# Optimization experiments

Measured on AMD Instinct MI355X. Metric: run time of the kernel, lower is better.

Reference implementation:

```python
import jax, jax.numpy as jnp
import numpy as np
from functools import partial

FRAME_RATE = 100
MIN_BPM = 55.0
MAX_BPM = 215.0
THRESHOLD = 0.05
TRANSITION_LAMBDA = 100.0  # madmom-style exponential tempo-change penalty
NEG = jnp.float32(-1e9)


def _build_dbn():
    """Bar-pointer DBN: one block of `tau` phase states per tempo interval tau."""
    min_int = int(round(60.0 * FRAME_RATE / MAX_BPM))
    max_int = int(round(60.0 * FRAME_RATE / MIN_BPM))
    intervals = np.arange(min_int, max_int + 1)              # (T_tempi,)
    state_positions = np.concatenate([np.arange(t) for t in intervals])  # (S,)
    first_idx = np.cumsum(intervals) - intervals             # pos-0 state per tempo
    last_idx = np.cumsum(intervals) - 1                      # last state per tempo
    # exponential tempo-transition distribution, row-normalized in log space
    ratio = intervals[None, :].astype(np.float64) / intervals[:, None]
    raw = -TRANSITION_LAMBDA * np.abs(ratio - 1.0)
    trans_log = raw - np.log(np.exp(raw - raw.max(1, keepdims=True)).sum(1, keepdims=True)) - raw.max(1, keepdims=True)
    return (
        jnp.asarray(state_positions == 0),                    # pos0_mask (S,) bool
        jnp.asarray(first_idx, dtype=jnp.int32),
        jnp.asarray(last_idx, dtype=jnp.int32),
        jnp.asarray(trans_log, dtype=jnp.float32),            # (T_tempi, T_tempi)
    )


def setup_inputs() -> dict:
    key = jax.random.key(0)
    logit = jax.random.normal(key, (4, 6000), dtype=jnp.float32)
    return {"logit": logit}


@jax.jit
def reference(logit):
    pos0_mask, first_idx, last_idx, trans_log = _build_dbn()
    S = pos0_mask.shape[0]
    B, T = logit.shape

    beat_lp = jax.nn.log_sigmoid(logit)      # (B, T)
    nonbeat_lp = jax.nn.log_sigmoid(-logit)  # (B, T)

    def emission(b_t, nb_t):
        # (B, S): beat log-prob on phase-0 states, non-beat elsewhere
        return jnp.where(pos0_mask[None, :], b_t[:, None], nb_t[:, None])

    # ---- Viterbi forward pass with backpointers ----
    def step(delta, xs):
        b_t, nb_t = xs
        prev_last = delta[:, last_idx]                         # (B, T_tempi)
        cand = prev_last[:, :, None] + trans_log[None, :, :]   # (B, from, to)
        from_beat = cand.max(axis=1)                           # (B, T_tempi)
        bp_beat = last_idx[cand.argmax(axis=1)]                # (B, T_tempi)
        # within-tempo advance: state s comes from s-1 (blocks are contiguous)
        shifted = jnp.concatenate(
            [jnp.full((B, 1), NEG, delta.dtype), delta[:, :-1]], axis=1)
        combined = shifted.at[:, first_idx].set(from_beat)
        new_delta = combined + emission(b_t, nb_t)
        bp = jnp.broadcast_to(jnp.arange(S, dtype=jnp.int32) - 1, (B, S))
        bp = bp.at[:, first_idx].set(bp_beat)
        return new_delta, bp

    delta0 = emission(beat_lp[:, 0], nonbeat_lp[:, 0]) - jnp.log(jnp.float32(S))
    xs = (beat_lp[:, 1:].T, nonbeat_lp[:, 1:].T)               # each (T-1, B)
    delta_final, bps = jax.lax.scan(step, delta0, xs)          # bps: (T-1, B, S)

    # ---- backtrack ----
    final_state = jnp.argmax(delta_final, axis=1).astype(jnp.int32)  # (B,)

    def back(state, bp_t):
        prev = jnp.take_along_axis(bp_t, state[:, None], axis=1)[:, 0]
        return prev, state

    state0, ys = jax.lax.scan(back, final_state, bps, reverse=True)
    path = jnp.concatenate([state0[None, :], ys], axis=0)      # (T, B) state ids

    on_beat = pos0_mask[path].T                                # (B, T)
    act = jax.nn.sigmoid(logit)
    beat_mask = on_beat & (act >= jnp.float32(THRESHOLD))
    return beat_mask.astype(jnp.float32)                       # 1.0 at beat frames
```

## Files before the change

### kernel.cpp

```cpp
#include <hip/hip_runtime.h>
#include <math.h>

#define NTAU 82
#define TMIN 28
#define S_TOT 5617
#define TF 6000
#define BATCH 4
#define WMAX 28
#define AP 84
#define LP 96
#define GP 88
#define NTHREADS 1024
#define NCHUNK 215
#define CHUNK_G (WMAX * GP)
#define NPOS 41
#define FLAG_STRIDE 64

#define TRANS_OFF 0
#define BLP_OFF   8192
#define NBLP_OFF  32768
#define AH_OFF    57344
#define FLAG_OFF  (AH_OFF + BATCH * NCHUNK * CHUNK_G)
#define RESV_OFF  (FLAG_OFF + 8 * FLAG_STRIDE)
#define RESI_OFF  (RESV_OFF + 8)

typedef float v2f __attribute__((ext_vector_type(2)));

__device__ __forceinline__ int first_of(int b) { return b * (55 + b) / 2; }

__device__ __forceinline__ float logsig(float x) {
    return -(fmaxf(-x, 0.0f) + log1pf(expf(-fabsf(x))));
}

__global__ void k_trans(float* __restrict__ ws) {
    int i = blockIdx.x;
    int j = threadIdx.x;
    __shared__ double sh[128];
    double raw = 0.0, e = 0.0;
    double ti = 28.0 + (double)i;
    if (j < NTAU) {
        double tj = 28.0 + (double)j;
        raw = -100.0 * fabs(tj / ti - 1.0);
        e = exp(raw);
    }
    sh[j] = e;
    __syncthreads();
    for (int st = 64; st > 0; st >>= 1) {
        if (j < st) sh[j] += sh[j + st];
        __syncthreads();
    }
    double lse = log(sh[0]);
    if (j < NTAU) ws[TRANS_OFF + i * NTAU + j] = (float)(raw - lse);
}

__global__ void k_emis(const float* __restrict__ logit, float* __restrict__ ws,
                       float* __restrict__ out) {
    int idx = blockIdx.x * blockDim.x + threadIdx.x;
    if (idx < BATCH * TF) {
        float x = logit[idx];
        ws[BLP_OFF + idx]  = logsig(x);
        ws[NBLP_OFF + idx] = logsig(-x);
        out[idx] = 0.0f;
    }
}

__global__ void k_flags(int* __restrict__ flags) {
    int i = blockIdx.x * blockDim.x + threadIdx.x;
    if (i < 8 * FLAG_STRIDE) flags[i] = 0;
}

__global__ void k_ahpad(float* __restrict__ Ah) {
    int i = blockIdx.x * blockDim.x + threadIdx.x;
    const int total = BATCH * NCHUNK * WMAX * 2 * 3;
    if (i < total) {
        int c3 = i % 3; int rest = i / 3;
        int par = rest & 1; rest >>= 1;
        int row = rest % WMAX; rest /= WMAX;
        int chunk = rest % NCHUNK; int bb = rest / NCHUNK;
        Ah[(size_t)bb * NCHUNK * CHUNK_G + (size_t)chunk * CHUNK_G
           + row * GP + par * 44 + 41 + c3] = -1.0e30f;
    }
}

__global__ __attribute__((amdgpu_flat_work_group_size(NTHREADS, NTHREADS),
                          amdgpu_waves_per_eu(4, 4),
                          amdgpu_num_vgpr(128)))
void k_viterbi(const float* __restrict__ logit,
               const float* __restrict__ transg,
               const float* __restrict__ blp_all,
               const float* __restrict__ nblp_all,
               float* __restrict__ Ah_all,
               int*   __restrict__ flags,
               float* __restrict__ resv,
               int*   __restrict__ resi,
               float* __restrict__ out) {
    const int tid = threadIdx.x;
    const int b   = blockIdx.x >> 1;
    const int h   = blockIdx.x & 1;

    const float* blp  = blp_all  + b * TF;
    const float* nblp = nblp_all + b * TF;
    float* Ah = Ah_all + (size_t)b * (NCHUNK * CHUNK_G);
    int* flagOut = flags + (b * 2 + h) * FLAG_STRIDE;
    int* flagIn  = flags + (b * 2 + (1 - h)) * FLAG_STRIDE;

    __shared__ float V[2832];
    __shared__ __align__(16) float A_lds[WMAX * LP];
    __shared__ __align__(16) float fb[CHUNK_G];
    __shared__ __align__(16) float win_nb[4][WMAX];
    __shared__ __align__(16) float win_b[4][WMAX];
    __shared__ float wv[16];
    __shared__ int   wi[16];
    __shared__ int   sstate;

    const int iseg = tid & 3;
    const int jpp  = (tid >> 2) % 21;
    const int tg   = tid / 84;
    const bool p2act = (tid < 1008);
    const int p0s = iseg * 12;
    const int j0 = 4 * jpp + h;
    const bool j1v = (jpp < 20);
    const int j1 = j1v ? (4 * jpp + 2 + h) : j0;

    float trO0[12], trO1[12], trP0[12], trP1[12];
#pragma unroll
    for (int k = 0; k < 12; ++k) {
        trO0[k] = -1.0e30f; trO1[k] = -1.0e30f;
        trP0[k] = -1.0e30f; trP1[k] = -1.0e30f;
    }
    if (p2act) {
#pragma unroll
        for (int k = 0; k < 12; ++k) {
            const int p = p0s + k;
            if (p <= 40) {
                const int iO = 2 * p + h, iP = 2 * p + 1 - h;
                trO0[k] = transg[iO * NTAU + j0];
                trP0[k] = transg[iP * NTAU + j0];
                if (j1v) {
                    trO1[k] = transg[iO * NTAU + j1];
                    trP1[k] = transg[iP * NTAU + j1];
                }
            }
        }
    }

    const bool ract = (tid < 1008);
    const int ro = ract ? (tid / 36) : 27;
    const int sp = tid % 36;
    const bool rv2 = ract && (sp < 5);
    const int pA = sp, pB = sp + 36;
    const int tauA = 28 + 2 * pA + h, tauB = 28 + 2 * pB + h;
    const int foA = pA * (27 + pA + h), foB = pB * (27 + pB + h);
    int rrA = ro, rrB = ro;

    const int NF_TOT = NPOS * (NPOS - 1 + h);
    int nrR[2], nrFo[2], nrTau[2];
    bool nrV[2];
#pragma unroll
    for (int q = 0; q < 2; ++q) {
        const int f = tid + q * NTHREADS;
        nrV[q] = (f < NF_TOT);
        nrR[q] = 28; nrFo[q] = 0; nrTau[q] = 109;
        if (nrV[q]) {
            int lo = 0, hi = NPOS - 1;
            while (lo < hi) { int mid = (lo + hi + 1) >> 1;
                              if (mid * (mid - 1 + h) <= f) lo = mid; else hi = mid - 1; }
            const int m = f - lo * (lo - 1 + h);
            nrR[q]   = TMIN + m;
            nrFo[q]  = lo * (27 + lo + h);
            nrTau[q] = TMIN + 2 * lo + h;
        }
    }

    const float logS = (float)log((double)S_TOT);
    const float b0 = blp[0], n0 = nblp[0];
    const int SOWN = NPOS * (68 + h);
    for (int g = tid; g < SOWN; g += NTHREADS) {
        int lo = 0, hi = NPOS - 1;
        while (lo < hi) { int mid = (lo + hi + 1) >> 1;
                          if (mid * (27 + mid + h) <= g) lo = mid; else hi = mid - 1; }
        const int tau = TMIN + 2 * lo + h;
        const int r = g - lo * (27 + lo + h);
        V[g] = ((r == tau - 1) ? b0 : n0) - logS;
    }

    for (int idx = tid; idx < WMAX * LP; idx += NTHREADS) A_lds[idx] = -1.0e30f;

    auto winload = [&](int cc) {
        if (cc < NCHUNK && tid < WMAX) {
            int gt = 1 + cc * WMAX + tid;
            win_nb[cc & 3][tid] = (gt < TF) ? nblp[gt] : 0.0f;
            win_b [cc & 3][tid] = (gt < TF) ? blp[gt]  : 0.0f;
        }
    };
    winload(0);
    winload(1);
    __syncthreads();

#define PH2P(av, aw, t0a, t0b, t1a, t1b) { \
    float x0 = (av) + (t0a); float y0 = (aw) + (t0b); \
    m0 = fmaxf(fmaxf(m0, x0), y0); \
    float x1 = (av) + (t1a); float y1 = (aw) + (t1b); \
    m1 = fmaxf(fmaxf(m1, x1), y1); }

    float cvA = 0.0f, cvB = 0.0f;
    float pm0[3], pm1[3];
    for (int c = 0; c < NCHUNK; ++c) {
        const int buf = c & 3;
        float* AhC = Ah + (size_t)c * CHUNK_G;

        cvA = ract ? V[foA + rrA] : 0.0f;
        cvB = rv2  ? V[foB + rrB] : 0.0f;
        for (int tt = 0; tt < ro; ++tt) {
            const float w = win_nb[buf][tt];
            cvA += w; cvB += w;
        }
        if (ract) {
            A_lds[ro * LP + h * 48 + pA] = cvA;
            __hip_atomic_store(&AhC[ro * GP + h * 44 + pA], cvA,
                               __ATOMIC_RELAXED, __HIP_MEMORY_SCOPE_AGENT);
            if (rv2) {
                A_lds[ro * LP + h * 48 + pB] = cvB;
                __hip_atomic_store(&AhC[ro * GP + h * 44 + pB], cvB,
                                   __ATOMIC_RELAXED, __HIP_MEMORY_SCOPE_AGENT);
            }
        }
        winload(c + 2);
        __syncthreads();

        if (tid == 0)
            __hip_atomic_store(flagOut, c + 1, __ATOMIC_RELAXED, __HIP_MEMORY_SCOPE_AGENT);

        if (p2act) {
#pragma unroll
            for (int u = 0; u < 3; ++u) {
                const int tl = tg + 12 * u;
                float m0 = -INFINITY, m1 = -INFINITY;
                if (tl < WMAX) {
                    const float4* ar4 = (const float4*)&A_lds[tl * LP + h * 48 + p0s];
                    const float4 a0 = ar4[0], a1 = ar4[1], a2 = ar4[2];
                    PH2P(a0.x, a0.y, trO0[0], trO0[1], trO1[0], trO1[1])
                    PH2P(a0.z, a0.w, trO0[2], trO0[3], trO1[2], trO1[3])
                    PH2P(a1.x, a1.y, trO0[4], trO0[5], trO1[4], trO1[5])
                    PH2P(a1.z, a1.w, trO0[6], trO0[7], trO1[6], trO1[7])
                    PH2P(a2.x, a2.y, trO0[8], trO0[9], trO1[8], trO1[9])
                    PH2P(a2.z, a2.w, trO0[10], trO0[11], trO1[10], trO1[11])
                }
                pm0[u] = m0; pm1[u] = m1;
            }
        }

        {
            const int a0 = nrFo[0] + nrR[0];
            const int a1 = nrV[1] ? (nrFo[1] + nrR[1]) : a0;
            v2f v01 = v2f{V[a0], V[a1]};
#pragma unroll
            for (int tt = 0; tt < WMAX; ++tt) {
                const float w = win_nb[buf][tt];
                v01 += v2f{w, w};
            }
            V[a0] = v01.x;
            if (nrV[1]) V[a1] = v01.y;
        }

        if (tid == 0) {
            int guard = 0;
            while (__hip_atomic_load(flagIn, __ATOMIC_RELAXED, __HIP_MEMORY_SCOPE_AGENT) < c + 1) {
                __builtin_amdgcn_s_sleep(1);
                if (++guard > (1 << 24)) break;
            }
        }
        __syncthreads();

        if (tid < 308) {
            const int row = tid / 11, s4 = tid % 11;
            const float4 v4 = *(const float4*)&AhC[row * GP + (1 - h) * 44 + s4 * 4];
            *(float4*)&A_lds[row * LP + (1 - h) * 48 + s4 * 4] = v4;
        }
        __syncthreads();

        if (p2act) {
#pragma unroll
            for (int u = 0; u < 3; ++u) {
                const int tl = tg + 12 * u;
                if (tl < WMAX) {
                    const float4* ar4 = (const float4*)&A_lds[tl * LP + (1 - h) * 48 + p0s];
                    const float4 a0 = ar4[0], a1 = ar4[1], a2 = ar4[2];
                    float m0 = pm0[u], m1 = pm1[u];
                    PH2P(a0.x, a0.y, trP0[0], trP0[1], trP1[0], trP1[1])
                    PH2P(a0.z, a0.w, trP0[2], trP0[3], trP1[2], trP1[3])
                    PH2P(a1.x, a1.y, trP0[4], trP0[5], trP1[4], trP1[5])
                    PH2P(a1.z, a1.w, trP0[6], trP0[7], trP1[6], trP1[7])
                    PH2P(a2.x, a2.y, trP0[8], trP0[9], trP1[8], trP1[9])
                    PH2P(a2.z, a2.w, trP0[10], trP0[11], trP1[10], trP1[11])
                    m0 = fmaxf(m0, __shfl_xor(m0, 1)); m1 = fmaxf(m1, __shfl_xor(m1, 1));
                    m0 = fmaxf(m0, __shfl_xor(m0, 2)); m1 = fmaxf(m1, __shfl_xor(m1, 2));
                    if (iseg == 0) {
                        fb[tl * AP + j0] = m0;
                        if (j1v) fb[tl * AP + j1] = m1;
                    }
                }
            }
        }
        __syncthreads();

        {
            const int colA = 2 * pA + h, colB = 2 * pB + h;
            const float bw = win_b[buf][ro];
            float eA = ract ? (fb[ro * AP + colA] + bw) : 0.0f;
            float eB = rv2  ? (fb[ro * AP + colB] + bw) : 0.0f;
            for (int tt = ro + 1; tt < WMAX; ++tt) {
                const float w = win_nb[buf][tt];
                eA += w; eB += w;
            }
            const bool keepC = (c == NCHUNK - 1) && (ro >= 7);
            if (ract) {
                V[foA + rrA] = keepC ? cvA : eA;
                if (rv2) V[foB + rrB] = keepC ? cvB : eB;
            }
            rrA += WMAX; if (rrA >= tauA) rrA -= tauA;
            rrB += WMAX; if (rrB >= tauB) rrB -= tauB;
        }
#pragma unroll
        for (int q = 0; q < 2; ++q) {
            if (nrV[q]) { nrR[q] += WMAX; if (nrR[q] >= nrTau[q]) nrR[q] -= nrTau[q]; }
        }
        __syncthreads();
    }
#undef PH2P

    float bvv = -INFINITY; int bss = 0x7fffffff;
    for (int g = tid; g < SOWN; g += NTHREADS) {
        int lo = 0, hi = NPOS - 1;
        while (lo < hi) { int mid = (lo + hi + 1) >> 1;
                          if (mid * (27 + mid + h) <= g) lo = mid; else hi = mid - 1; }
        const int tau = TMIN + 2 * lo + h;
        const int r = g - lo * (27 + lo + h);
        const int p = (5998 - r) % tau;
        const int s = first_of(2 * lo + h) + p;
        const float v = V[g];
        if (v > bvv || (v == bvv && s < bss)) { bvv = v; bss = s; }
    }
#pragma unroll
    for (int d = 1; d < 64; d <<= 1) {
        float ov = __shfl_xor(bvv, d);
        int   os = __shfl_xor(bss, d);
        if (ov > bvv || (ov == bvv && os < bss)) { bvv = ov; bss = os; }
    }
    if ((tid & 63) == 0) { wv[tid >> 6] = bvv; wi[tid >> 6] = bss; }
    __syncthreads();

    if (tid == 0) {
        float bv = wv[0]; int bs = wi[0];
#pragma unroll
        for (int k = 1; k < 16; ++k) {
            if (wv[k] > bv || (wv[k] == bv && wi[k] < bs)) { bv = wv[k]; bs = wi[k]; }
        }
        resv[b * 2 + h] = bv;
        resi[b * 2 + h] = bs;
        __hip_atomic_fetch_add(flagOut, 1, __ATOMIC_RELEASE, __HIP_MEMORY_SCOPE_AGENT);
        wv[0] = bv; wi[0] = bs;
    }
    if (h == 1) return;
    __syncthreads();

    if (tid == 0) {
        int guard = 0;
        while (__hip_atomic_load(flagIn, __ATOMIC_RELAXED, __HIP_MEMORY_SCOPE_AGENT) < NCHUNK + 1) {
            __builtin_amdgcn_s_sleep(1);
            if (++guard > (1 << 26)) break;
        }
        int fv = __hip_atomic_load(flagIn, __ATOMIC_ACQUIRE, __HIP_MEMORY_SCOPE_AGENT);
        if (fv == -0x7fffffff) wv[1] = -1.0e30f;
        float bv = wv[0]; int bs = wi[0];
        const float pv = resv[b * 2 + 1];
        const int   ps = resi[b * 2 + 1];
        if (pv > bv || (pv == bv && ps < bs)) { bv = pv; bs = ps; }
        sstate = bs;
    }
    __syncthreads();

    if (tid < 64) {
        const int lane = tid;
        int s = sstate;
        int t = TF - 1;
        for (int guard = 0; guard < 400; ++guard) {
            int lo = 0, hi = NTAU - 1;
            while (lo < hi) { int mid = (lo + hi + 1) >> 1;
                              if (first_of(mid) <= s) lo = mid; else hi = mid - 1; }
            int j = lo;
            int p = s - first_of(j);
            int tb = t - p;
            if (tb < 0) break;
            if (lane == 0) {
                float x = logit[b * TF + tb];
                float act = 1.0f / (1.0f + expf(-x));
                if (act >= 0.05f) out[b * TF + tb] = 1.0f;
            }
            if (tb == 0) break;
            const int tq = tb - 1;
            const float* arow = Ah + (size_t)(tq / WMAX) * CHUNK_G + (tq % WMAX) * GP;
            float cvv = arow[(lane & 1) * 44 + (lane >> 1)] + transg[lane * NTAU + j];
            int ci = lane;
            if (lane < NTAU - 64) {
                const int i2 = 64 + lane;
                float c2 = arow[(i2 & 1) * 44 + (i2 >> 1)] + transg[i2 * NTAU + j];
                if (c2 > cvv) { cvv = c2; ci = i2; }
            }
#pragma unroll
            for (int d = 1; d < 64; d <<= 1) {
                float ov = __shfl_xor(cvv, d, 64);
                int   oi = __shfl_xor(ci, d, 64);
                if (ov > cvv || (ov == cvv && oi < ci)) { cvv = ov; ci = oi; }
            }
            s = first_of(ci) + (TMIN + ci) - 1;
            t = tb - 1;
        }
    }
}

extern "C" void kernel_launch(void* const* d_in, const int* in_sizes, int n_in,
                              void* d_out, int out_size, void* d_ws, size_t ws_size,
                              hipStream_t stream) {
    const float* logit = (const float*)d_in[0];
    float* out = (float*)d_out;
    float* ws = (float*)d_ws;
    k_trans<<<dim3(NTAU), dim3(128), 0, stream>>>(ws);
    k_emis<<<dim3((BATCH * TF + 255) / 256), dim3(256), 0, stream>>>(logit, ws, out);
    k_flags<<<dim3(2), dim3(256), 0, stream>>>((int*)(ws + FLAG_OFF));
    k_ahpad<<<dim3((BATCH * NCHUNK * WMAX * 2 * 3 + 255) / 256), dim3(256), 0, stream>>>(ws + AH_OFF);
    k_viterbi<<<dim3(BATCH * 2), dim3(NTHREADS), 0, stream>>>(
        logit, ws + TRANS_OFF, ws + BLP_OFF, ws + NBLP_OFF, ws + AH_OFF,
        (int*)(ws + FLAG_OFF), ws + RESV_OFF, (int*)(ws + RESI_OFF), out);
}
```

Measured before the change: 1.250 ms.

## Merge split-tempo workgroup pairs into one workgroup per batch, removing cross-block flags

Replaces the two-workgroups-per-batch split, where each block owned half the tempo states and exchanged chunk boundary values through global memory with spin-wait flags, with a single 1024-thread workgroup per batch that keeps all states in LDS. This removes the per-chunk inter-block handshake, the global reload of the partner's values, and the flag and padding init kernels. In exchange each thread does more max-plus work (22 from-tempi per thread) and only 4 workgroups run, so per-block compute and register pressure rise.

New measurement: 1.596 ms. +27.7%, slower.

```diff
diff --git a/kernel.cpp b/kernel.cpp
--- a/kernel.cpp
+++ b/kernel.cpp
@@ -8,25 +8,20 @@
 #define BATCH 4
 #define WMAX 28
 #define AP 84
-#define LP 96
-#define GP 88
 #define NTHREADS 1024
 #define NCHUNK 215
-#define CHUNK_G (WMAX * GP)
-#define NPOS 41
-#define FLAG_STRIDE 64
+#define CHUNK_G (WMAX * AP)
+#define NCAP (WMAX * NTAU)
+#define NNR 3321
 
 #define TRANS_OFF 0
 #define BLP_OFF   8192
 #define NBLP_OFF  32768
 #define AH_OFF    57344
-#define FLAG_OFF  (AH_OFF + BATCH * NCHUNK * CHUNK_G)
-#define RESV_OFF  (FLAG_OFF + 8 * FLAG_STRIDE)
-#define RESI_OFF  (RESV_OFF + 8)
 
 typedef float v2f __attribute__((ext_vector_type(2)));
 
-__device__ __forceinline__ int first_of(int b) { return b * (55 + b) / 2; }
+__device__ __forceinline__ int first_of(int bb) { return bb * (55 + bb) / 2; }
 
 __device__ __forceinline__ float logsig(float x) {
     return -(fmaxf(-x, 0.0f) + log1pf(expf(-fabsf(x))));
@@ -64,48 +59,23 @@
     }
 }
 
-__global__ void k_flags(int* __restrict__ flags) {
-    int i = blockIdx.x * blockDim.x + threadIdx.x;
-    if (i < 8 * FLAG_STRIDE) flags[i] = 0;
-}
-
-__global__ void k_ahpad(float* __restrict__ Ah) {
-    int i = blockIdx.x * blockDim.x + threadIdx.x;
-    const int total = BATCH * NCHUNK * WMAX * 2 * 3;
-    if (i < total) {
-        int c3 = i % 3; int rest = i / 3;
-        int par = rest & 1; rest >>= 1;
-        int row = rest % WMAX; rest /= WMAX;
-        int chunk = rest % NCHUNK; int bb = rest / NCHUNK;
-        Ah[(size_t)bb * NCHUNK * CHUNK_G + (size_t)chunk * CHUNK_G
-           + row * GP + par * 44 + 41 + c3] = -1.0e30f;
-    }
-}
-
 __global__ __attribute__((amdgpu_flat_work_group_size(NTHREADS, NTHREADS),
-                          amdgpu_waves_per_eu(4, 4),
-                          amdgpu_num_vgpr(128)))
+                          amdgpu_waves_per_eu(4, 4)))
 void k_viterbi(const float* __restrict__ logit,
                const float* __restrict__ transg,
                const float* __restrict__ blp_all,
                const float* __restrict__ nblp_all,
                float* __restrict__ Ah_all,
-               int*   __restrict__ flags,
-               float* __restrict__ resv,
-               int*   __restrict__ resi,
                float* __restrict__ out) {
     const int tid = threadIdx.x;
-    const int b   = blockIdx.x >> 1;
-    const int h   = blockIdx.x & 1;
+    const int b   = blockIdx.x;
 
     const float* blp  = blp_all  + b * TF;
     const float* nblp = nblp_all + b * TF;
     float* Ah = Ah_all + (size_t)b * (NCHUNK * CHUNK_G);
-    int* flagOut = flags + (b * 2 + h) * FLAG_STRIDE;
-    int* flagIn  = flags + (b * 2 + (1 - h)) * FLAG_STRIDE;
-
-    __shared__ float V[2832];
-    __shared__ __align__(16) float A_lds[WMAX * LP];
+
+    __shared__ float V[S_TOT];
+    __shared__ __align__(16) float A_lds[CHUNK_G];
     __shared__ __align__(16) float fb[CHUNK_G];
     __shared__ __align__(16) float win_nb[4][WMAX];
     __shared__ __align__(16) float win_b[4][WMAX];
@@ -114,81 +84,76 @@
     __shared__ int   sstate;
 
     const int iseg = tid & 3;
-    const int jpp  = (tid >> 2) % 21;
-    const int tg   = tid / 84;
-    const bool p2act = (tid < 1008);
-    const int p0s = iseg * 12;
-    const int j0 = 4 * jpp + h;
-    const bool j1v = (jpp < 20);
-    const int j1 = j1v ? (4 * jpp + 2 + h) : j0;
-
-    float trO0[12], trO1[12], trP0[12], trP1[12];
-#pragma unroll
-    for (int k = 0; k < 12; ++k) {
-        trO0[k] = -1.0e30f; trO1[k] = -1.0e30f;
-        trP0[k] = -1.0e30f; trP1[k] = -1.0e30f;
-    }
+    const int jp   = (tid >> 2) % 41;
+    const int rg   = tid / 164;
+    const bool p2act = (tid < 984);
+    const int ib = iseg * 20;
+    const int j0 = 2 * jp;
+
+    float tr0[22], tr1[22];
+#pragma unroll
+    for (int k = 0; k < 22; ++k) { tr0[k] = -1.0e30f; tr1[k] = -1.0e30f; }
     if (p2act) {
 #pragma unroll
-        for (int k = 0; k < 12; ++k) {
-            const int p = p0s + k;
-            if (p <= 40) {
-                const int iO = 2 * p + h, iP = 2 * p + 1 - h;
-                trO0[k] = transg[iO * NTAU + j0];
-                trP0[k] = transg[iP * NTAU + j0];
-                if (j1v) {
-                    trO1[k] = transg[iO * NTAU + j1];
-                    trP1[k] = transg[iP * NTAU + j1];
-                }
-            }
-        }
-    }
-
-    const bool ract = (tid < 1008);
-    const int ro = ract ? (tid / 36) : 27;
-    const int sp = tid % 36;
-    const bool rv2 = ract && (sp < 5);
-    const int pA = sp, pB = sp + 36;
-    const int tauA = 28 + 2 * pA + h, tauB = 28 + 2 * pB + h;
-    const int foA = pA * (27 + pA + h), foB = pB * (27 + pB + h);
-    int rrA = ro, rrB = ro;
-
-    const int NF_TOT = NPOS * (NPOS - 1 + h);
-    int nrR[2], nrFo[2], nrTau[2];
-    bool nrV[2];
-#pragma unroll
-    for (int q = 0; q < 2; ++q) {
+        for (int k = 0; k < 22; ++k) {
+            tr0[k] = transg[(ib + k) * NTAU + j0];
+            tr1[k] = transg[(ib + k) * NTAU + j0 + 1];
+        }
+    }
+
+    int cro[3], coff[3], cva[3], clim[3], ctau[3];
+    bool cvalid[3];
+#pragma unroll
+    for (int q = 0; q < 3; ++q) {
+        const int slot = tid + q * NTHREADS;
+        cvalid[q] = (slot < NCAP);
+        if (cvalid[q]) {
+            const int ro  = slot / NTAU;
+            const int blk = slot - ro * NTAU;
+            const int fo  = first_of(blk);
+            cro[q]  = ro;
+            coff[q] = ro * AP + blk;
+            cva[q]  = fo + ro;
+            ctau[q] = TMIN + blk;
+            clim[q] = fo + ctau[q];
+        } else {
+            cro[q] = 0; coff[q] = 0; cva[q] = 0; ctau[q] = TMIN; clim[q] = TMIN;
+        }
+    }
+
+    int nva[4], nlim[4], ntau[4];
+    bool nvalid[4];
+#pragma unroll
+    for (int q = 0; q < 4; ++q) {
         const int f = tid + q * NTHREADS;
-        nrV[q] = (f < NF_TOT);
-        nrR[q] = 28; nrFo[q] = 0; nrTau[q] = 109;
-        if (nrV[q]) {
-            int lo = 0, hi = NPOS - 1;
+        nvalid[q] = (f < NNR);
+        if (nvalid[q]) {
+            int lo = 1, hi = NTAU - 1;
             while (lo < hi) { int mid = (lo + hi + 1) >> 1;
-                              if (mid * (mid - 1 + h) <= f) lo = mid; else hi = mid - 1; }
-            const int m = f - lo * (lo - 1 + h);
-            nrR[q]   = TMIN + m;
-            nrFo[q]  = lo * (27 + lo + h);
-            nrTau[q] = TMIN + 2 * lo + h;
+                              if (mid * (mid - 1) / 2 <= f) lo = mid; else hi = mid - 1; }
+            const int m  = f - lo * (lo - 1) / 2;
+            const int fo = first_of(lo);
+            nva[q]  = fo + TMIN + m;
+            ntau[q] = TMIN + lo;
+            nlim[q] = fo + ntau[q];
+        } else {
+            nva[q] = 0; ntau[q] = TMIN; nlim[q] = TMIN;
         }
     }
 
     const float logS = (float)log((double)S_TOT);
     const float b0 = blp[0], n0 = nblp[0];
-    const int SOWN = NPOS * (68 + h);
-    for (int g = tid; g < SOWN; g += NTHREADS) {
-        int lo = 0, hi = NPOS - 1;
+    for (int g = tid; g < S_TOT; g += NTHREADS) {
+        int lo = 0, hi = NTAU - 1;
         while (lo < hi) { int mid = (lo + hi + 1) >> 1;
-                          if (mid * (27 + mid + h) <= g) lo = mid; else hi = mid - 1; }
-        const int tau = TMIN + 2 * lo + h;
-        const int r = g - lo * (27 + lo + h);
-        V[g] = ((r == tau - 1) ? b0 : n0) - logS;
-    }
-
-    for (int idx = tid; idx < WMAX * LP; idx += NTHREADS) A_lds[idx] = -1.0e30f;
+                          if (first_of(mid) <= g) lo = mid; else hi = mid - 1; }
+        const int r = g - first_of(lo);
+        V[g] = ((r == TMIN + lo - 1) ? b0 : n0) - logS;
+    }
 
     auto winload = [&](int cc) {
         if (cc < NCHUNK && tid < WMAX) {
-            int gt = 1 + cc * WMAX + tid;
+            const int gt = 1 + cc * WMAX + tid;
             win_nb[cc & 3][tid] = (gt < TF) ? nblp[gt] : 0.0f;
             win_b [cc & 3][tid] = (gt < TF) ? blp[gt]  : 0.0f;
         }
@@ -203,179 +168,121 @@
     float x1 = (av) + (t1a); float y1 = (aw) + (t1b); \
     m1 = fmaxf(fmaxf(m1, x1), y1); }
 
-    float cvA = 0.0f, cvB = 0.0f;
-    float pm0[3], pm1[3];
+    float cv[3];
     for (int c = 0; c < NCHUNK; ++c) {
         const int buf = c & 3;
         float* AhC = Ah + (size_t)c * CHUNK_G;
 
-        cvA = ract ? V[foA + rrA] : 0.0f;
-        cvB = rv2  ? V[foB + rrB] : 0.0f;
-        for (int tt = 0; tt < ro; ++tt) {
-            const float w = win_nb[buf][tt];
-            cvA += w; cvB += w;
-        }
-        if (ract) {
-            A_lds[ro * LP + h * 48 + pA] = cvA;
-            __hip_atomic_store(&AhC[ro * GP + h * 44 + pA], cvA,
-                               __ATOMIC_RELAXED, __HIP_MEMORY_SCOPE_AGENT);
-            if (rv2) {
-                A_lds[ro * LP + h * 48 + pB] = cvB;
-                __hip_atomic_store(&AhC[ro * GP + h * 44 + pB], cvB,
-                                   __ATOMIC_RELAXED, __HIP_MEMORY_SCOPE_AGENT);
-            }
-        }
         winload(c + 2);
+
+#pragma unroll
+        for (int q = 0; q < 3; ++q) {
+            float s = V[cva[q]];
+            const int ro = cro[q];
+            for (int tt = 0; tt < ro; ++tt) s += win_nb[buf][tt];
+            cv[q] = s;
+            if (cvalid[q]) A_lds[coff[q]] = s;
+        }
         __syncthreads();
 
-        if (tid == 0)
-            __hip_atomic_store(flagOut, c + 1, __ATOMIC_RELAXED, __HIP_MEMORY_SCOPE_AGENT);
+#pragma unroll
+        for (int q = 0; q < 3; ++q)
+            if (cvalid[q]) AhC[coff[q]] = cv[q];
 
         if (p2act) {
 #pragma unroll
-            for (int u = 0; u < 3; ++u) {
-                const int tl = tg + 12 * u;
-                float m0 = -INFINITY, m1 = -INFINITY;
+            for (int u = 0; u < 5; ++u) {
+                const int tl = rg + 6 * u;
                 if (tl < WMAX) {
-                    const float4* ar4 = (const float4*)&A_lds[tl * LP + h * 48 + p0s];
-                    const float4 a0 = ar4[0], a1 = ar4[1], a2 = ar4[2];
-                    PH2P(a0.x, a0.y, trO0[0], trO0[1], trO1[0], trO1[1])
-                    PH2P(a0.z, a0.w, trO0[2], trO0[3], trO1[2], trO1[3])
-                    PH2P(a1.x, a1.y, trO0[4], trO0[5], trO1[4], trO1[5])
-                    PH2P(a1.z, a1.w, trO0[6], trO0[7], trO1[6], trO1[7])
-                    PH2P(a2.x, a2.y, trO0[8], trO0[9], trO1[8], trO1[9])
-                    PH2P(a2.z, a2.w, trO0[10], trO0[11], trO1[10], trO1[11])
+                    const float* ar = &A_lds[tl * AP + ib];
+                    const float4 a0 = ((const float4*)ar)[0];
+                    const float4 a1 = ((const float4*)ar)[1];
+                    const float4 a2 = ((const float4*)ar)[2];
+                    const float4 a3 = ((const float4*)ar)[3];
+                    const float4 a4 = ((const float4*)ar)[4];
+                    const v2f    a5 = *(const v2f*)(ar + 20);
+                    float m0 = -INFINITY, m1 = -INFINITY;
+                    PH2P(a0.x, a0.y, tr0[0],  tr0[1],  tr1[0],  tr1[1])
+                    PH2P(a0.z, a0.w, tr0[2],  tr0[3],  tr1[2],  tr1[3])
+                    PH2P(a1.x, a1.y, tr0[4],  tr0[5],  tr1[4],  tr1[5])
+                    PH2P(a1.z, a1.w, tr0[6],  tr0[7],  tr1[6],  tr1[7])
+                    PH2P(a2.x, a2.y, tr0[8],  tr0[9],  tr1[8],  tr1[9])
+                    PH2P(a2.z, a2.w, tr0[10], tr0[11], tr1[10], tr1[11])
+                    PH2P(a3.x, a3.y, tr0[12], tr0[13], tr1[12], tr1[13])
+                    PH2P(a3.z, a3.w, tr0[14], tr0[15], tr1[14], tr1[15])
+                    PH2P(a4.x, a4.y, tr0[16], tr0[17], tr1[16], tr1[17])
+                    PH2P(a4.z, a4.w, tr0[18], tr0[19], tr1[18], tr1[19])
+                    PH2P(a5.x, a5.y, tr0[20], tr0[21], tr1[20], tr1[21])
+                    m0 = fmaxf(m0, __shfl_xor(m0, 1));
+                    m1 = fmaxf(m1, __shfl_xor(m1, 1));
+                    m0 = fmaxf(m0, __shfl_xor(m0, 2));
+                    m1 = fmaxf(m1, __shfl_xor(m1, 2));
+                    if (iseg == 0) *(v2f*)&fb[tl * AP + j0] = v2f{m0, m1};
                 }
-                pm0[u] = m0; pm1[u] = m1;
             }
         }
 
         {
-            const int a0 = nrFo[0] + nrR[0];
-            const int a1 = nrV[1] ? (nrFo[1] + nrR[1]) : a0;
-            v2f v01 = v2f{V[a0], V[a1]};
+            v2f x01 = v2f{V[nva[0]], V[nva[1]]};
+            v2f x23 = v2f{V[nva[2]], V[nva[3]]};
 #pragma unroll
             for (int tt = 0; tt < WMAX; ++tt) {
                 const float w = win_nb[buf][tt];
-                v01 += v2f{w, w};
-            }
-            V[a0] = v01.x;
-            if (nrV[1]) V[a1] = v01.y;
-        }
-
-        if (tid == 0) {
-            int guard = 0;
-            while (__hip_atomic_load(flagIn, __ATOMIC_RELAXED, __HIP_MEMORY_SCOPE_AGENT) < c + 1) {
-                __builtin_amdgcn_s_sleep(1);
-                if (++guard > (1 << 24)) break;
-            }
+                x01 += v2f{w, w};
+                x23 += v2f{w, w};
+            }
+            V[nva[0]] = x01.x;
+            V[nva[1]] = x01.y;
+            V[nva[2]] = x23.x;
+            if (nvalid[3]) V[nva[3]] = x23.y;
         }
         __syncthreads();
 
-        if (tid < 308) {
-            const int row = tid / 11, s4 = tid % 11;
-            const float4 v4 = *(const float4*)&AhC[row * GP + (1 - h) * 44 + s4 * 4];
-            *(float4*)&A_lds[row * LP + (1 - h) * 48 + s4 * 4] = v4;
+#pragma unroll
+        for (int q = 0; q < 3; ++q) {
+            if (cvalid[q]) {
+                const int ro = cro[q];
+                float e = fb[coff[q]] + win_b[buf][ro];
+                for (int tt = ro + 1; tt < WMAX; ++tt) e += win_nb[buf][tt];
+                const bool keepC = (c == NCHUNK - 1) && (ro >= 7);
+                V[cva[q]] = keepC ? cv[q] : e;
+            }
+            cva[q] += WMAX; if (cva[q] >= clim[q]) cva[q] -= ctau[q];
+        }
+#pragma unroll
+        for (int q = 0; q < 4; ++q) {
+            nva[q] += WMAX; if (nva[q] >= nlim[q]) nva[q] -= ntau[q];
         }
         __syncthreads();
-
-        if (p2act) {
-#pragma unroll
-            for (int u = 0; u < 3; ++u) {
-                const int tl = tg + 12 * u;
-                if (tl < WMAX) {
-                    const float4* ar4 = (const float4*)&A_lds[tl * LP + (1 - h) * 48 + p0s];
-                    const float4 a0 = ar4[0], a1 = ar4[1], a2 = ar4[2];
-                    float m0 = pm0[u], m1 = pm1[u];
-                    PH2P(a0.x, a0.y, trP0[0], trP0[1], trP1[0], trP1[1])
-                    PH2P(a0.z, a0.w, trP0[2], trP0[3], trP1[2], trP1[3])
-                    PH2P(a1.x, a1.y, trP0[4], trP0[5], trP1[4], trP1[5])
-                    PH2P(a1.z, a1.w, trP0[6], trP0[7], trP1[6], trP1[7])
-                    PH2P(a2.x, a2.y, trP0[8], trP0[9], trP1[8], trP1[9])
-                    PH2P(a2.z, a2.w, trP0[10], trP0[11], trP1[10], trP1[11])
-                    m0 = fmaxf(m0, __shfl_xor(m0, 1)); m1 = fmaxf(m1, __shfl_xor(m1, 1));
-                    m0 = fmaxf(m0, __shfl_xor(m0, 2)); m1 = fmaxf(m1, __shfl_xor(m1, 2));
-                    if (iseg == 0) {
-                        fb[tl * AP + j0] = m0;
-                        if (j1v) fb[tl * AP + j1] = m1;
-                    }
-                }
-            }
-        }
-        __syncthreads();
-
-        {
-            const int colA = 2 * pA + h, colB = 2 * pB + h;
-            const float bw = win_b[buf][ro];
-            float eA = ract ? (fb[ro * AP + colA] + bw) : 0.0f;
-            float eB = rv2  ? (fb[ro * AP + colB] + bw) : 0.0f;
-            for (int tt = ro + 1; tt < WMAX; ++tt) {
-                const float w = win_nb[buf][tt];
-                eA += w; eB += w;
-            }
-            const bool keepC = (c == NCHUNK - 1) && (ro >= 7);
-            if (ract) {
-                V[foA + rrA] = keepC ? cvA : eA;
-                if (rv2) V[foB + rrB] = keepC ? cvB : eB;
-            }
-            rrA += WMAX; if (rrA >= tauA) rrA -= tauA;
-            rrB += WMAX; if (rrB >= tauB) rrB -= tauB;
-        }
-#pragma unroll
-        for (int q = 0; q < 2; ++q) {
-            if (nrV[q]) { nrR[q] += WMAX; if (nrR[q] >= nrTau[q]) nrR[q] -= nrTau[q]; }
-        }
-        __syncthreads();
     }
 #undef PH2P
 
     float bvv = -INFINITY; int bss = 0x7fffffff;
-    for (int g = tid; g < SOWN; g += NTHREADS) {
-        int lo = 0, hi = NPOS - 1;
+    for (int g = tid; g < S_TOT; g += NTHREADS) {
+        int lo = 0, hi = NTAU - 1;
         while (lo < hi) { int mid = (lo + hi + 1) >> 1;
-                          if (mid * (27 + mid + h) <= g) lo = mid; else hi = mid - 1; }
-        const int tau = TMIN + 2 * lo + h;
-        const int r = g - lo * (27 + lo + h);
-        const int p = (5998 - r) % tau;
-        const int s = first_of(2 * lo + h) + p;
+                          if (first_of(mid) <= g) lo = mid; else hi = mid - 1; }
+        const int fo  = first_of(lo);
+        const int r   = g - fo;
+        const int tau = TMIN + lo;
+        const int p   = (5998 - r) % tau;
+        const int s   = fo + p;
         const float v = V[g];
         if (v > bvv || (v == bvv && s < bss)) { bvv = v; bss = s; }
     }
 #pragma unroll
     for (int d = 1; d < 64; d <<= 1) {
-        float ov = __shfl_xor(bvv, d);
-        int   os = __shfl_xor(bss, d);
+        const float ov = __shfl_xor(bvv, d);
+        const int   os = __shfl_xor(bss, d);
         if (ov > bvv || (ov == bvv && os < bss)) { bvv = ov; bss = os; }
     }
     if ((tid & 63) == 0) { wv[tid >> 6] = bvv; wi[tid >> 6] = bss; }
     __syncthreads();
-
     if (tid == 0) {
         float bv = wv[0]; int bs = wi[0];
 #pragma unroll
-        for (int k = 1; k < 16; ++k) {
+        for (int k = 1; k < 16; ++k)
             if (wv[k] > bv || (wv[k] == bv && wi[k] < bs)) { bv = wv[k]; bs = wi[k]; }
-        }
-        resv[b * 2 + h] = bv;
-        resi[b * 2 + h] = bs;
-        __hip_atomic_fetch_add(flagOut, 1, __ATOMIC_RELEASE, __HIP_MEMORY_SCOPE_AGENT);
-        wv[0] = bv; wi[0] = bs;
-    }
-    if (h == 1) return;
-    __syncthreads();
-
-    if (tid == 0) {
-        int guard = 0;
-        while (__hip_atomic_load(flagIn, __ATOMIC_RELAXED, __HIP_MEMORY_SCOPE_AGENT) < NCHUNK + 1) {
-            __builtin_amdgcn_s_sleep(1);
-            if (++guard > (1 << 26)) break;
-        }
-        int fv = __hip_atomic_load(flagIn, __ATOMIC_ACQUIRE, __HIP_MEMORY_SCOPE_AGENT);
-        if (fv == -0x7fffffff) wv[1] = -1.0e30f;
-        float bv = wv[0]; int bs = wi[0];
-        const float pv = resv[b * 2 + 1];
-        const int   ps = resi[b * 2 + 1];
-        if (pv > bv || (pv == bv && ps < bs)) { bv = pv; bs = ps; }
         sstate = bs;
     }
     __syncthreads();
@@ -388,29 +295,29 @@
             int lo = 0, hi = NTAU - 1;
             while (lo < hi) { int mid = (lo + hi + 1) >> 1;
                               if (first_of(mid) <= s) lo = mid; else hi = mid - 1; }
-            int j = lo;
-            int p = s - first_of(j);
-            int tb = t - p;
+            const int j = lo;
+            const int p = s - first_of(j);
+            const int tb = t - p;
             if (tb < 0) break;
             if (lane == 0) {
-                float x = logit[b * TF + tb];
-                float act = 1.0f / (1.0f + expf(-x));
+                const float x = logit[b * TF + tb];
+                const float act = 1.0f / (1.0f + expf(-x));
                 if (act >= 0.05f) out[b * TF + tb] = 1.0f;
             }
             if (tb == 0) break;
             const int tq = tb - 1;
-            const float* arow = Ah + (size_t)(tq / WMAX) * CHUNK_G + (tq % WMAX) * GP;
-            float cvv = arow[(lane & 1) * 44 + (lane >> 1)] + transg[lane * NTAU + j];
+            const float* arow = Ah + (size_t)(tq / WMAX) * CHUNK_G + (tq % WMAX) * AP;
+            float cvv = arow[lane] + transg[lane * NTAU + j];
             int ci = lane;
             if (lane < NTAU - 64) {
                 const int i2 = 64 + lane;
-                float c2 = arow[(i2 & 1) * 44 + (i2 >> 1)] + transg[i2 * NTAU + j];
+                const float c2 = arow[i2] + transg[i2 * NTAU + j];
                 if (c2 > cvv) { cvv = c2; ci = i2; }
             }
 #pragma unroll
             for (int d = 1; d < 64; d <<= 1) {
-                float ov = __shfl_xor(cvv, d, 64);
-                int   oi = __shfl_xor(ci, d, 64);
+                const float ov = __shfl_xor(cvv, d, 64);
+                const int   oi = __shfl_xor(ci, d, 64);
                 if (ov > cvv || (ov == cvv && oi < ci)) { cvv = ov; ci = oi; }
             }
             s = first_of(ci) + (TMIN + ci) - 1;
@@ -427,9 +334,6 @@
     float* ws = (float*)d_ws;
     k_trans<<<dim3(NTAU), dim3(128), 0, stream>>>(ws);
     k_emis<<<dim3((BATCH * TF + 255) / 256), dim3(256), 0, stream>>>(logit, ws, out);
-    k_flags<<<dim3(2), dim3(256), 0, stream>>>((int*)(ws + FLAG_OFF));
-    k_ahpad<<<dim3((BATCH * NCHUNK * WMAX * 2 * 3 + 255) / 256), dim3(256), 0, stream>>>(ws + AH_OFF);
-    k_viterbi<<<dim3(BATCH * 2), dim3(NTHREADS), 0, stream>>>(
-        logit, ws + TRANS_OFF, ws + BLP_OFF, ws + NBLP_OFF, ws + AH_OFF,
-        (int*)(ws + FLAG_OFF), ws + RESV_OFF, (int*)(ws + RESI_OFF), out);
-}
+    k_viterbi<<<dim3(BATCH), dim3(NTHREADS), 0, stream>>>(
+        logit, ws + TRANS_OFF, ws + BLP_OFF, ws + NBLP_OFF, ws + AH_OFF, out);
+}
```

## Use per-wave cross-block flags, LDS-only barriers, and register-prefetched emission windows

Applied to the files above, without the earlier changes.

Replaces the single per-block progress flag, which needed a full __syncthreads before it could be set, with sixteen per-wave flags. Each wave publishes its flag once its own global stores drain, and the consumer polls all sixteen. Block barriers become LDS-only waits plus s_barrier, so outstanding global loads are not drained at each barrier, and the emission window is now prefetched into registers one chunk ahead. Final-result handoff moves to separate flags. Risks: correctness of the memory ordering rests on relaxed atomics plus explicit vmcnt waits, and the consumer now polls sixteen flags per chunk.

Result: slower. 1.423 ms (+13.9%).

```diff
diff --git a/kernel.cpp b/kernel.cpp
--- a/kernel.cpp
+++ b/kernel.cpp
@@ -21,7 +21,7 @@
 #define NBLP_OFF  32768
 #define AH_OFF    57344
 #define FLAG_OFF  (AH_OFF + BATCH * NCHUNK * CHUNK_G)
-#define RESV_OFF  (FLAG_OFF + 8 * FLAG_STRIDE)
+#define RESV_OFF  (FLAG_OFF + 16 * FLAG_STRIDE)
 #define RESI_OFF  (RESV_OFF + 8)
 
 typedef float v2f __attribute__((ext_vector_type(2)));
@@ -30,6 +30,13 @@
 
 __device__ __forceinline__ float logsig(float x) {
     return -(fmaxf(-x, 0.0f) + log1pf(expf(-fabsf(x))));
+}
+
+__device__ __forceinline__ void bar_lds() {
+    __builtin_amdgcn_sched_barrier(0);
+    asm volatile("s_waitcnt lgkmcnt(0)" ::: "memory");
+    __builtin_amdgcn_s_barrier();
+    __builtin_amdgcn_sched_barrier(0);
 }
 
 __global__ void k_trans(float* __restrict__ ws) {
@@ -66,7 +73,7 @@
 
 __global__ void k_flags(int* __restrict__ flags) {
     int i = blockIdx.x * blockDim.x + threadIdx.x;
-    if (i < 8 * FLAG_STRIDE) flags[i] = 0;
+    if (i < 16 * FLAG_STRIDE) flags[i] = 0;
 }
 
 __global__ void k_ahpad(float* __restrict__ Ah) {
@@ -101,8 +108,10 @@
     const float* blp  = blp_all  + b * TF;
     const float* nblp = nblp_all + b * TF;
     float* Ah = Ah_all + (size_t)b * (NCHUNK * CHUNK_G);
-    int* flagOut = flags + (b * 2 + h) * FLAG_STRIDE;
-    int* flagIn  = flags + (b * 2 + (1 - h)) * FLAG_STRIDE;
+    int* flagOut16 = flags + (b * 2 + h) * FLAG_STRIDE;
+    int* flagIn16  = flags + (b * 2 + (1 - h)) * FLAG_STRIDE;
+    int* resFlagOut = flags + (8 + b * 2 + h) * FLAG_STRIDE;
+    int* resFlagIn  = flags + (8 + b * 2 + (1 - h)) * FLAG_STRIDE;
 
     __shared__ float V[2832];
     __shared__ __align__(16) float A_lds[WMAX * LP];
@@ -193,8 +202,23 @@
             win_b [cc & 3][tid] = (gt < TF) ? blp[gt]  : 0.0f;
         }
     };
+    float rg_nb = 0.0f, rg_b = 0.0f;
+    auto win_issue = [&](int cc) {
+        if (cc < NCHUNK && tid < WMAX) {
+            int gt = 1 + cc * WMAX + tid;
+            rg_nb = (gt < TF) ? nblp[gt] : 0.0f;
+            rg_b  = (gt < TF) ? blp[gt]  : 0.0f;
+        }
+    };
+    auto win_commit = [&](int cc) {
+        if (cc < NCHUNK && tid < WMAX) {
+            win_nb[cc & 3][tid] = rg_nb;
+            win_b [cc & 3][tid] = rg_b;
+        }
+    };
     winload(0);
     winload(1);
+    win_issue(2);
     __syncthreads();
 
 #define PH2P(av, aw, t0a, t0b, t1a, t1b) { \
@@ -203,6 +227,7 @@
     float x1 = (av) + (t1a); float y1 = (aw) + (t1b); \
     m1 = fmaxf(fmaxf(m1, x1), y1); }
 
+    const int wvid = tid >> 6;
     float cvA = 0.0f, cvB = 0.0f;
     float pm0[3], pm1[3];
     for (int c = 0; c < NCHUNK; ++c) {
@@ -225,11 +250,9 @@
                                    __ATOMIC_RELAXED, __HIP_MEMORY_SCOPE_AGENT);
             }
         }
-        winload(c + 2);
-        __syncthreads();
-
-        if (tid == 0)
-            __hip_atomic_store(flagOut, c + 1, __ATOMIC_RELAXED, __HIP_MEMORY_SCOPE_AGENT);
+        bar_lds();
+
+        win_commit(c + 2);
 
         if (p2act) {
 #pragma unroll
@@ -250,6 +273,14 @@
             }
         }
 
+        __builtin_amdgcn_sched_barrier(0);
+        asm volatile("s_waitcnt vmcnt(0)" ::: "memory");
+        if ((tid & 63) == 0)
+            __hip_atomic_store(&flagOut16[wvid], c + 1,
+                               __ATOMIC_RELAXED, __HIP_MEMORY_SCOPE_AGENT);
+
+        win_issue(c + 3);
+
         {
             const int a0 = nrFo[0] + nrR[0];
             const int a1 = nrV[1] ? (nrFo[1] + nrR[1]) : a0;
@@ -263,21 +294,22 @@
             if (nrV[1]) V[a1] = v01.y;
         }
 
-        if (tid == 0) {
+        if (tid < 16) {
             int guard = 0;
-            while (__hip_atomic_load(flagIn, __ATOMIC_RELAXED, __HIP_MEMORY_SCOPE_AGENT) < c + 1) {
+            while (__hip_atomic_load(&flagIn16[tid], __ATOMIC_RELAXED,
+                                     __HIP_MEMORY_SCOPE_AGENT) < c + 1) {
                 __builtin_amdgcn_s_sleep(1);
                 if (++guard > (1 << 24)) break;
             }
         }
-        __syncthreads();
+        bar_lds();
 
         if (tid < 308) {
             const int row = tid / 11, s4 = tid % 11;
             const float4 v4 = *(const float4*)&AhC[row * GP + (1 - h) * 44 + s4 * 4];
             *(float4*)&A_lds[row * LP + (1 - h) * 48 + s4 * 4] = v4;
         }
-        __syncthreads();
+        bar_lds();
 
         if (p2act) {
 #pragma unroll
@@ -302,7 +334,7 @@
                 }
             }
         }
-        __syncthreads();
+        bar_lds();
 
         {
             const int colA = 2 * pA + h, colB = 2 * pB + h;
@@ -325,7 +357,7 @@
         for (int q = 0; q < 2; ++q) {
             if (nrV[q]) { nrR[q] += WMAX; if (nrR[q] >= nrTau[q]) nrR[q] -= nrTau[q]; }
         }
-        __syncthreads();
+        bar_lds();
     }
 #undef PH2P
 
@@ -358,7 +390,7 @@
         }
         resv[b * 2 + h] = bv;
         resi[b * 2 + h] = bs;
-        __hip_atomic_fetch_add(flagOut, 1, __ATOMIC_RELEASE, __HIP_MEMORY_SCOPE_AGENT);
+        __hip_atomic_fetch_add(resFlagOut, 1, __ATOMIC_RELEASE, __HIP_MEMORY_SCOPE_AGENT);
         wv[0] = bv; wi[0] = bs;
     }
     if (h == 1) return;
@@ -366,11 +398,11 @@
 
     if (tid == 0) {
         int guard = 0;
-        while (__hip_atomic_load(flagIn, __ATOMIC_RELAXED, __HIP_MEMORY_SCOPE_AGENT) < NCHUNK + 1) {
+        while (__hip_atomic_load(resFlagIn, __ATOMIC_RELAXED, __HIP_MEMORY_SCOPE_AGENT) < 1) {
             __builtin_amdgcn_s_sleep(1);
             if (++guard > (1 << 26)) break;
         }
-        int fv = __hip_atomic_load(flagIn, __ATOMIC_ACQUIRE, __HIP_MEMORY_SCOPE_AGENT);
+        int fv = __hip_atomic_load(resFlagIn, __ATOMIC_ACQUIRE, __HIP_MEMORY_SCOPE_AGENT);
         if (fv == -0x7fffffff) wv[1] = -1.0e30f;
         float bv = wv[0]; int bs = wi[0];
         const float pv = resv[b * 2 + 1];
@@ -427,7 +459,7 @@
     float* ws = (float*)d_ws;
     k_trans<<<dim3(NTAU), dim3(128), 0, stream>>>(ws);
     k_emis<<<dim3((BATCH * TF + 255) / 256), dim3(256), 0, stream>>>(logit, ws, out);
-    k_flags<<<dim3(2), dim3(256), 0, stream>>>((int*)(ws + FLAG_OFF));
+    k_flags<<<dim3(4), dim3(256), 0, stream>>>((int*)(ws + FLAG_OFF));
     k_ahpad<<<dim3((BATCH * NCHUNK * WMAX * 2 * 3 + 255) / 256), dim3(256), 0, stream>>>(ws + AH_OFF);
     k_viterbi<<<dim3(BATCH * 2), dim3(NTHREADS), 0, stream>>>(
         logit, ws + TRANS_OFF, ws + BLP_OFF, ws + NBLP_OFF, ws + AH_OFF,
```

## Place paired Viterbi blocks on same XCD and use plain stores when co-located

Applied to the files above, without the earlier changes.

Launches 16 blocks and discards half, so each batch's two half-blocks (w and w+8) are likely placed on the same XCD under round-robin dispatch. Each block reads its XCC ID and exchanges it with its partner. When both are on the same XCD, the per-step inter-block data exchange uses plain stores instead of agent-scope atomic stores, aiming to keep communication in the shared L2 and lower cross-die latency. The cost is a startup handshake spin-wait and a dependence on undocumented block-to-XCD placement. Memory-ordering correctness with plain stores relies on the flag protocol that follows.

Result: faster. 1.225 ms (median of 2 runs) (-2.0%).

```diff
diff --git a/kernel.cpp b/kernel.cpp
--- a/kernel.cpp
+++ b/kernel.cpp
@@ -21,7 +21,7 @@
 #define NBLP_OFF  32768
 #define AH_OFF    57344
 #define FLAG_OFF  (AH_OFF + BATCH * NCHUNK * CHUNK_G)
-#define RESV_OFF  (FLAG_OFF + 8 * FLAG_STRIDE)
+#define RESV_OFF  (FLAG_OFF + 16 * FLAG_STRIDE)
 #define RESI_OFF  (RESV_OFF + 8)
 
 typedef float v2f __attribute__((ext_vector_type(2)));
@@ -66,7 +66,7 @@
 
 __global__ void k_flags(int* __restrict__ flags) {
     int i = blockIdx.x * blockDim.x + threadIdx.x;
-    if (i < 8 * FLAG_STRIDE) flags[i] = 0;
+    if (i < 16 * FLAG_STRIDE) flags[i] = 0;
 }
 
 __global__ void k_ahpad(float* __restrict__ Ah) {
@@ -95,14 +95,18 @@
                int*   __restrict__ resi,
                float* __restrict__ out) {
     const int tid = threadIdx.x;
-    const int b   = blockIdx.x >> 1;
-    const int h   = blockIdx.x & 1;
+    const int w   = blockIdx.x;
+    if ((w & 7) >= 4) return;
+    const int b   = w & 3;
+    const int h   = w >> 3;
 
     const float* blp  = blp_all  + b * TF;
     const float* nblp = nblp_all + b * TF;
     float* Ah = Ah_all + (size_t)b * (NCHUNK * CHUNK_G);
     int* flagOut = flags + (b * 2 + h) * FLAG_STRIDE;
     int* flagIn  = flags + (b * 2 + (1 - h)) * FLAG_STRIDE;
+    int* xslotOut = flags + (8 + b * 2 + h) * FLAG_STRIDE;
+    int* xslotIn  = flags + (8 + b * 2 + (1 - h)) * FLAG_STRIDE;
 
     __shared__ float V[2832];
     __shared__ __align__(16) float A_lds[WMAX * LP];
@@ -112,6 +116,7 @@
     __shared__ float wv[16];
     __shared__ int   wi[16];
     __shared__ int   sstate;
+    __shared__ int   s_samex;
 
     const int iseg = tid & 3;
     const int jpp  = (tid >> 2) % 21;
@@ -195,7 +200,21 @@
     };
     winload(0);
     winload(1);
+
+    if (tid == 0) {
+        int myx;
+        asm volatile("s_getreg_b32 %0, hwreg(HW_REG_XCC_ID, 0, 4)" : "=s"(myx));
+        __hip_atomic_store(xslotOut, myx + 1, __ATOMIC_RELAXED, __HIP_MEMORY_SCOPE_AGENT);
+        int px = 0, guard = 0;
+        while ((px = __hip_atomic_load(xslotIn, __ATOMIC_RELAXED,
+                                       __HIP_MEMORY_SCOPE_AGENT)) == 0) {
+            __builtin_amdgcn_s_sleep(1);
+            if (++guard > (1 << 24)) break;
+        }
+        s_samex = (px == myx + 1) ? 1 : 0;
+    }
     __syncthreads();
+    const bool samex = (s_samex != 0);
 
 #define PH2P(av, aw, t0a, t0b, t1a, t1b) { \
     float x0 = (av) + (t0a); float y0 = (aw) + (t0b); \
@@ -217,12 +236,20 @@
         }
         if (ract) {
             A_lds[ro * LP + h * 48 + pA] = cvA;
-            __hip_atomic_store(&AhC[ro * GP + h * 44 + pA], cvA,
-                               __ATOMIC_RELAXED, __HIP_MEMORY_SCOPE_AGENT);
+            if (samex) {
+                AhC[ro * GP + h * 44 + pA] = cvA;
+            } else {
+                __hip_atomic_store(&AhC[ro * GP + h * 44 + pA], cvA,
+                                   __ATOMIC_RELAXED, __HIP_MEMORY_SCOPE_AGENT);
+            }
             if (rv2) {
                 A_lds[ro * LP + h * 48 + pB] = cvB;
-                __hip_atomic_store(&AhC[ro * GP + h * 44 + pB], cvB,
-                                   __ATOMIC_RELAXED, __HIP_MEMORY_SCOPE_AGENT);
+                if (samex) {
+                    AhC[ro * GP + h * 44 + pB] = cvB;
+                } else {
+                    __hip_atomic_store(&AhC[ro * GP + h * 44 + pB], cvB,
+                                       __ATOMIC_RELAXED, __HIP_MEMORY_SCOPE_AGENT);
+                }
             }
         }
         winload(c + 2);
@@ -427,9 +454,9 @@
     float* ws = (float*)d_ws;
     k_trans<<<dim3(NTAU), dim3(128), 0, stream>>>(ws);
     k_emis<<<dim3((BATCH * TF + 255) / 256), dim3(256), 0, stream>>>(logit, ws, out);
-    k_flags<<<dim3(2), dim3(256), 0, stream>>>((int*)(ws + FLAG_OFF));
+    k_flags<<<dim3(4), dim3(256), 0, stream>>>((int*)(ws + FLAG_OFF));
     k_ahpad<<<dim3((BATCH * NCHUNK * WMAX * 2 * 3 + 255) / 256), dim3(256), 0, stream>>>(ws + AH_OFF);
-    k_viterbi<<<dim3(BATCH * 2), dim3(NTHREADS), 0, stream>>>(
+    k_viterbi<<<dim3(16), dim3(NTHREADS), 0, stream>>>(
         logit, ws + TRANS_OFF, ws + BLP_OFF, ws + NBLP_OFF, ws + AH_OFF,
         (int*)(ws + FLAG_OFF), ws + RESV_OFF, (int*)(ws + RESI_OFF), out);
 }
```
